# Kernel optimization log

Hardware: AMD Instinct MI355X
Metric: run time of the kernel (lower is better)

## Reference

```python
import jax, jax.numpy as jnp
import numpy as np

L, ND, ED = 1024, 64, 32  # seq len, node_embedding_dim, edge_embedding_dim
LN_EPS = 1e-5  # haiku LayerNorm default


def setup_inputs() -> dict:
    key = jax.random.key(0)
    ks = jax.random.split(key, 8)
    node_features = jax.random.normal(ks[0], (L, ND), dtype=jnp.float32)
    pair_features = jax.random.normal(ks[1], (L, L, ED), dtype=jnp.float32)
    # hk.Linear(ED) over concat([node_i, node_j, pair]) -> fan_in = 2*ND + ED
    fan_pair = 2 * ND + ED
    W_pair = jax.random.normal(ks[2], (fan_pair, ED), dtype=jnp.float32) / np.sqrt(fan_pair)
    b_pair = jnp.zeros((ED,), dtype=jnp.float32)
    # hk.Linear(ND) over concat([node, pair_to_node]) -> fan_in = ND + ED
    fan_node = ND + ED
    W_node = jax.random.normal(ks[3], (fan_node, ND), dtype=jnp.float32) / np.sqrt(fan_node)
    b_node = jnp.zeros((ND,), dtype=jnp.float32)
    ln_scale = jnp.ones((ND,), dtype=jnp.float32)
    ln_offset = jnp.zeros((ND,), dtype=jnp.float32)
    return {
        "node_features": node_features,
        "pair_features": pair_features,
        "W_pair": W_pair,
        "b_pair": b_pair,
        "W_node": W_node,
        "b_node": b_node,
        "ln_scale": ln_scale,
        "ln_offset": ln_offset,
    }


def reference(node_features, pair_features, W_pair, b_pair, W_node, b_node, ln_scale, ln_offset):
    # Pair update: Linear(concat([bcast node_i, bcast node_j, pair])).
    # Split the weight into node_i / node_j / pair blocks so we never
    # materialize the (L, L, 2*ND+ED) concat tensor -- same math.
    Wi = W_pair[:ND]          # (ND, ED)
    Wj = W_pair[ND:2 * ND]    # (ND, ED)
    Wp = W_pair[2 * ND:]      # (ED, ED)
    ni = node_features @ Wi   # (L, ED)
    nj = node_features @ Wj   # (L, ED)
    pair_update = (ni[:, None, :] + nj[None, :, :]
                   + jnp.einsum('ije,ef->ijf', pair_features, Wp) + b_pair)
    pair_out = pair_features + pair_update                      # (L, L, ED)

    # Node update: mean over axis=1, concat, linear, residual, LayerNorm.
    pair_to_node = jnp.mean(pair_out, axis=1)                   # (L, ED)
    node_in = jnp.concatenate([node_features, pair_to_node], axis=-1)  # (L, ND+ED)
    node = node_features + node_in @ W_node + b_node            # (L, ND)

    mean = jnp.mean(node, axis=-1, keepdims=True)
    var = jnp.var(node, axis=-1, keepdims=True)
    node = (node - mean) * jax.lax.rsqrt(var + LN_EPS) * ln_scale + ln_offset
    return node, pair_out
```

## Files before the change

kernel.cpp:

```cpp
#include <hip/hip_runtime.h>
#include <stdint.h>

#define LSEQ 1024
#define EDIM 32
#define NDIM 64

typedef __attribute__((ext_vector_type(8))) short short8;
typedef __attribute__((ext_vector_type(4))) float f32x4;

static __device__ __forceinline__ unsigned short f2bf(float f) {
    unsigned int u = __float_as_uint(f);
    u += 0x7FFFu + ((u >> 16) & 1u);
    return (unsigned short)(u >> 16);
}

__global__ __launch_bounds__(256) void evo_pre(
    const float* __restrict__ node,
    const float* __restrict__ Wpair,
    const float* __restrict__ bpair,
    float* __restrict__ niB,
    float* __restrict__ njB,
    unsigned short* __restrict__ wpT)
{
    int g = blockIdx.x * 256 + threadIdx.x;
    if (g < LSEQ * EDIM) {
        int i = g >> 5, f = g & 31;
        float acci = bpair[f];
        float accj = 0.0f;
        const float* nrow = node + i * NDIM;
        #pragma unroll
        for (int k = 0; k < NDIM; ++k) {
            float nv = nrow[k];
            acci += nv * Wpair[k * 32 + f];
            accj += nv * Wpair[(64 + k) * 32 + f];
        }
        niB[g] = acci;
        njB[g] = accj;
    } else {
        int idx = g - LSEQ * EDIM;
        if (idx < EDIM * EDIM) {
            int f = idx >> 5, e = idx & 31;
            float v = Wpair[(128 + e) * 32 + f];
            if (e == f) v += 1.0f;
            wpT[f * 32 + e] = f2bf(v);
        }
    }
}

__global__ __launch_bounds__(256, 4) void evo_main(
    const float* __restrict__ pair,
    const float* __restrict__ niB,
    const float* __restrict__ njB,
    const unsigned short* __restrict__ wpT,
    float* __restrict__ partial,
    float* __restrict__ out_pair)
{
    __shared__ float tin[4][512];
    __shared__ float stage[4][512];
    __shared__ float red[4][32];

    const int blk  = blockIdx.x;
    const int i    = blk >> 1;
    const int h    = blk & 1;
    const int tid  = threadIdx.x;
    const int wave = tid >> 6;
    const int lane = tid & 63;
    const int c    = lane & 15;
    const int a    = lane >> 4;
    const int q    = lane & 7;
    const int r0   = lane >> 3;

    const short8 af0 = *(const short8*)(wpT + c * 32 + a * 8);
    const short8 af1 = *(const short8*)(wpT + (c + 16) * 32 + a * 8);
    const f32x4 ni_d = *(const f32x4*)(niB + i * 32 + q * 4);

    const int jw = (h << 9) + (wave << 7);
    const size_t tb = ((size_t)i * 1024 + (size_t)jw) * 32;
    const float* pinD = pair + tb + lane * 4;
    const float* njD  = njB + (size_t)(jw + r0) * 32 + q * 4;
    float*       preg = out_pair + tb + lane * 4;

    const int xin = (q ^ (r0 & 7)) * 4;
    float* inW0 = &tin[wave][r0 * 32 + xin];
    float* inW1 = inW0 + 256;
    const float* bf0p = &tin[wave][c * 32 + (((2 * a)     ^ (c & 7)) * 4)];
    const float* bf1p = &tin[wave][c * 32 + (((2 * a + 1) ^ (c & 7)) * 4)];

    const int key = (c & 7) << 2;
    float* wr0 = &stage[wave][c * 32 + ((4 * a) ^ key)];
    float* wr1 = &stage[wave][c * 32 + ((16 + 4 * a) ^ key)];
    const float* rd0 = &stage[wave][r0 * 32 + ((q * 4) ^ ((r0 & 7) << 2))];
    const float* rd1 = rd0 + 256;

    f32x4 P0[2], P1[2], J0[2], J1[2];
    P0[0] = *(const f32x4*)(pinD);
    P1[0] = *(const f32x4*)(pinD + 256);
    J0[0] = *(const f32x4*)(njD);
    J1[0] = *(const f32x4*)(njD + 256);

    f32x4 sumd = {0.f, 0.f, 0.f, 0.f};

    #pragma unroll
    for (int t = 0; t < 8; ++t) {
        const int cur = t & 1, nxt = cur ^ 1;
        if (t < 7) {
            P0[nxt] = *(const f32x4*)(pinD + (t + 1) * 512);
            P1[nxt] = *(const f32x4*)(pinD + (t + 1) * 512 + 256);
            J0[nxt] = *(const f32x4*)(njD + (t + 1) * 512);
            J1[nxt] = *(const f32x4*)(njD + (t + 1) * 512 + 256);
        }

        *(f32x4*)inW0 = P0[cur];
        *(f32x4*)inW1 = P1[cur];

        const f32x4 b0 = *(const f32x4*)bf0p;
        const f32x4 b1 = *(const f32x4*)bf1p;
        short8 bfrag;
        bfrag[0] = (short)f2bf(b0.x); bfrag[1] = (short)f2bf(b0.y);
        bfrag[2] = (short)f2bf(b0.z); bfrag[3] = (short)f2bf(b0.w);
        bfrag[4] = (short)f2bf(b1.x); bfrag[5] = (short)f2bf(b1.y);
        bfrag[6] = (short)f2bf(b1.z); bfrag[7] = (short)f2bf(b1.w);
        const f32x4 z = {0.f, 0.f, 0.f, 0.f};
        const f32x4 acc0 = __builtin_amdgcn_mfma_f32_16x16x32_bf16(af0, bfrag, z, 0, 0, 0);
        const f32x4 acc1 = __builtin_amdgcn_mfma_f32_16x16x32_bf16(af1, bfrag, z, 0, 0, 0);

        *(f32x4*)wr0 = acc0;
        *(f32x4*)wr1 = acc1;
        const f32x4 d0 = *(const f32x4*)rd0 + ni_d + J0[cur];
        const f32x4 d1 = *(const f32x4*)rd1 + ni_d + J1[cur];
        sumd += d0 + d1;
        *(f32x4*)(preg + t * 512)       = d0;
        *(f32x4*)(preg + t * 512 + 256) = d1;
    }

    for (int m = 8; m < 64; m <<= 1) {
        sumd.x += __shfl_xor(sumd.x, m);
        sumd.y += __shfl_xor(sumd.y, m);
        sumd.z += __shfl_xor(sumd.z, m);
        sumd.w += __shfl_xor(sumd.w, m);
    }
    if (lane < 8) *(f32x4*)&red[wave][q * 4] = sumd;
    __syncthreads();
    if (tid < 32) {
        partial[blk * 32 + tid] = red[0][tid] + red[1][tid] + red[2][tid] + red[3][tid];
    }
}

__global__ __launch_bounds__(64) void evo_finish(
    const float* __restrict__ node,
    const float* __restrict__ partial,
    const float* __restrict__ Wnode,
    const float* __restrict__ bnode,
    const float* __restrict__ lnsc,
    const float* __restrict__ lnof,
    float* __restrict__ out_node)
{
    __shared__ float node_f[64];
    __shared__ float p2n[32];
    const int i   = blockIdx.x;
    const int tid = threadIdx.x;

    node_f[tid] = node[i * 64 + tid];
    if (tid < 32) {
        p2n[tid] = (partial[(2 * i) * 32 + tid] + partial[(2 * i + 1) * 32 + tid])
                   * (1.0f / 1024.0f);
    }
    __syncthreads();

    float acc = node_f[tid] + bnode[tid];
    #pragma unroll 8
    for (int k = 0; k < 64; ++k)
        acc += node_f[k] * Wnode[k * 64 + tid];
    #pragma unroll 8
    for (int k = 0; k < 32; ++k)
        acc += p2n[k] * Wnode[(64 + k) * 64 + tid];

    float s = acc, s2 = acc * acc;
    for (int m = 1; m < 64; m <<= 1) {
        s  += __shfl_xor(s, m);
        s2 += __shfl_xor(s2, m);
    }
    const float mean = s * (1.0f / 64.0f);
    const float var  = s2 * (1.0f / 64.0f) - mean * mean;
    const float y = (acc - mean) * rsqrtf(var + 1e-5f) * lnsc[tid] + lnof[tid];
    out_node[i * 64 + tid] = y;
}

extern "C" void kernel_launch(void* const* d_in, const int* in_sizes, int n_in,
                              void* d_out, int out_size, void* d_ws, size_t ws_size,
                              hipStream_t stream) {
    const float* node  = (const float*)d_in[0];
    const float* pair  = (const float*)d_in[1];
    const float* Wpair = (const float*)d_in[2];
    const float* bpair = (const float*)d_in[3];
    const float* Wnode = (const float*)d_in[4];
    const float* bnode = (const float*)d_in[5];
    const float* lnsc  = (const float*)d_in[6];
    const float* lnof  = (const float*)d_in[7];

    float* niB = (float*)d_ws;
    float* njB = niB + LSEQ * EDIM;
    unsigned short* wpT = (unsigned short*)(njB + LSEQ * EDIM);
    float* partial = (float*)(wpT + EDIM * EDIM);

    float* out_node = (float*)d_out;
    float* out_pair = out_node + LSEQ * NDIM;

    evo_pre<<<132, 256, 0, stream>>>(node, Wpair, bpair, niB, njB, wpT);
    evo_main<<<2 * LSEQ, 256, 0, stream>>>(pair, niB, njB, wpT, partial, out_pair);
    evo_finish<<<LSEQ, 64, 0, stream>>>(node, partial, Wnode, bnode, lnsc, lnof,
                                        out_node);
}
```

Baseline: 60.64 us.

## Stream pair and nj tiles into LDS via async global_load_lds double buffering

```diff
diff --git a/kernel.cpp b/kernel.cpp
--- a/kernel.cpp
+++ b/kernel.cpp
@@ -12,6 +12,15 @@
     unsigned int u = __float_as_uint(f);
     u += 0x7FFFu + ((u >> 16) & 1u);
     return (unsigned short)(u >> 16);
+}
+
+static __device__ __forceinline__ void gll16(const float* g, float* l) {
+    __builtin_amdgcn_global_load_lds(
+        (const __attribute__((address_space(1))) void*)g,
+        (__attribute__((address_space(3))) void*)l, 16, 0, 0);
+}
+static __device__ __forceinline__ uint32_t ldsoff(const void* p) {
+    return (uint32_t)(uintptr_t)(const __attribute__((address_space(3))) void*)p;
 }
 
 __global__ __launch_bounds__(256) void evo_pre(
@@ -47,7 +56,7 @@
     }
 }
 
-__global__ __launch_bounds__(256, 4) void evo_main(
+__global__ __launch_bounds__(256, 3) void evo_main(
     const float* __restrict__ pair,
     const float* __restrict__ niB,
     const float* __restrict__ njB,
@@ -55,7 +64,8 @@
     float* __restrict__ partial,
     float* __restrict__ out_pair)
 {
-    __shared__ float tin[4][512];
+    __shared__ float pslot[4][2][512];
+    __shared__ float nslot[4][2][512];
     __shared__ float stage[4][512];
     __shared__ float red[4][32];
 
@@ -76,15 +86,13 @@
 
     const int jw = (h << 9) + (wave << 7);
     const size_t tb = ((size_t)i * 1024 + (size_t)jw) * 32;
-    const float* pinD = pair + tb + lane * 4;
-    const float* njD  = njB + (size_t)(jw + r0) * 32 + q * 4;
+
+    const float* psrc = pair + tb + r0 * 32 + (q ^ (r0 & 7)) * 4;
+    const float* nsrc = njB + (size_t)(jw + r0) * 32 + q * 4;
     float*       preg = out_pair + tb + lane * 4;
 
-    const int xin = (q ^ (r0 & 7)) * 4;
-    float* inW0 = &tin[wave][r0 * 32 + xin];
-    float* inW1 = inW0 + 256;
-    const float* bf0p = &tin[wave][c * 32 + (((2 * a)     ^ (c & 7)) * 4)];
-    const float* bf1p = &tin[wave][c * 32 + (((2 * a + 1) ^ (c & 7)) * 4)];
+    const int fi0 = c * 32 + (((2 * a)     ^ (c & 7)) << 2);
+    const int fi1 = c * 32 + (((2 * a + 1) ^ (c & 7)) << 2);
 
     const int key = (c & 7) << 2;
     float* wr0 = &stage[wave][c * 32 + ((4 * a) ^ key)];
@@ -92,29 +100,41 @@
     const float* rd0 = &stage[wave][r0 * 32 + ((q * 4) ^ ((r0 & 7) << 2))];
     const float* rd1 = rd0 + 256;
 
-    f32x4 P0[2], P1[2], J0[2], J1[2];
-    P0[0] = *(const f32x4*)(pinD);
-    P1[0] = *(const f32x4*)(pinD + 256);
-    J0[0] = *(const f32x4*)(njD);
-    J1[0] = *(const f32x4*)(njD + 256);
+    const uint32_t pb0 = ldsoff(&pslot[wave][0][0]);
+    const uint32_t pb1 = ldsoff(&pslot[wave][1][0]);
+    const uint32_t nb0 = ldsoff(&nslot[wave][0][0]);
+    const uint32_t nb1 = ldsoff(&nslot[wave][1][0]);
 
     f32x4 sumd = {0.f, 0.f, 0.f, 0.f};
+
+    __builtin_amdgcn_sched_barrier(0);
+    gll16(psrc,       &pslot[wave][0][0]);
+    gll16(psrc + 256, &pslot[wave][0][256]);
+    gll16(nsrc,       &nslot[wave][0][0]);
+    gll16(nsrc + 256, &nslot[wave][0][256]);
+    __builtin_amdgcn_sched_barrier(0);
+    gll16(psrc + 512, &pslot[wave][1][0]);
+    gll16(psrc + 768, &pslot[wave][1][256]);
+    gll16(nsrc + 512, &nslot[wave][1][0]);
+    gll16(nsrc + 768, &nslot[wave][1][256]);
 
     #pragma unroll
     for (int t = 0; t < 8; ++t) {
-        const int cur = t & 1, nxt = cur ^ 1;
-        if (t < 7) {
-            P0[nxt] = *(const f32x4*)(pinD + (t + 1) * 512);
-            P1[nxt] = *(const f32x4*)(pinD + (t + 1) * 512 + 256);
-            J0[nxt] = *(const f32x4*)(njD + (t + 1) * 512);
-            J1[nxt] = *(const f32x4*)(njD + (t + 1) * 512 + 256);
-        }
-
-        *(f32x4*)inW0 = P0[cur];
-        *(f32x4*)inW1 = P1[cur];
-
-        const f32x4 b0 = *(const f32x4*)bf0p;
-        const f32x4 b1 = *(const f32x4*)bf1p;
+        if (t == 0)      asm volatile("s_waitcnt vmcnt(4)" ::: "memory");
+        else if (t == 7) asm volatile("s_waitcnt vmcnt(2)" ::: "memory");
+        else             asm volatile("s_waitcnt vmcnt(6)" ::: "memory");
+        __builtin_amdgcn_sched_barrier(0);
+
+        const uint32_t pb = (t & 1) ? pb1 : pb0;
+        const uint32_t nb = (t & 1) ? nb1 : nb0;
+        f32x4 b0, b1, j0, j1;
+        asm volatile("ds_read_b128 %0, %1" : "=v"(b0) : "v"(pb + fi0 * 4));
+        asm volatile("ds_read_b128 %0, %1" : "=v"(b1) : "v"(pb + fi1 * 4));
+        asm volatile("ds_read_b128 %0, %1" : "=v"(j0) : "v"(nb + lane * 16));
+        asm volatile("ds_read_b128 %0, %1" : "=v"(j1) : "v"(nb + lane * 16 + 1024));
+        asm volatile("s_waitcnt lgkmcnt(0)" ::: "memory");
+        __builtin_amdgcn_sched_barrier(0);
+
         short8 bfrag;
         bfrag[0] = (short)f2bf(b0.x); bfrag[1] = (short)f2bf(b0.y);
         bfrag[2] = (short)f2bf(b0.z); bfrag[3] = (short)f2bf(b0.w);
@@ -126,11 +146,22 @@
 
         *(f32x4*)wr0 = acc0;
         *(f32x4*)wr1 = acc1;
-        const f32x4 d0 = *(const f32x4*)rd0 + ni_d + J0[cur];
-        const f32x4 d1 = *(const f32x4*)rd1 + ni_d + J1[cur];
+        const f32x4 d0 = *(const f32x4*)rd0 + ni_d + j0;
+        const f32x4 d1 = *(const f32x4*)rd1 + ni_d + j1;
         sumd += d0 + d1;
         *(f32x4*)(preg + t * 512)       = d0;
         *(f32x4*)(preg + t * 512 + 256) = d1;
+
+        if (t < 6) {
+            asm volatile("s_waitcnt lgkmcnt(0)" ::: "memory");
+            __builtin_amdgcn_sched_barrier(0);
+            float* pd = (t & 1) ? &pslot[wave][1][0] : &pslot[wave][0][0];
+            float* nd = (t & 1) ? &nslot[wave][1][0] : &nslot[wave][0][0];
+            gll16(psrc + (t + 2) * 512,       pd);
+            gll16(psrc + (t + 2) * 512 + 256, pd + 256);
+            gll16(nsrc + (t + 2) * 512,       nd);
+            gll16(nsrc + (t + 2) * 512 + 256, nd + 256);
+        }
     }
 
     for (int m = 8; m < 64; m <<= 1) {
```

After: 61.07 us. Within noise of the previous version (+0.7%).
